# Optimization experiments

Hardware: AMD Instinct MI355X
Metric: run time of the kernel (lower is better)

## Reference

```python
import jax, jax.numpy as jnp
import numpy as np

D = 1024
H = 4
HD = D // H
B = 256
L = 64
DILATIONS = (1, 4, 8, 16)


def setup_inputs() -> dict:
    key = jax.random.key(0)
    ks = jax.random.split(key, 12)
    s = 1.0 / np.sqrt(D)
    return {
        "x": jax.random.normal(ks[0], (B, D), jnp.float32),
        "hist": jax.random.normal(ks[1], (L, B, D), jnp.float32),
        "Wq": jax.random.normal(ks[2], (D, D), jnp.float32) * s,
        "bq": jnp.zeros((D,), jnp.float32),
        "Wk": jax.random.normal(ks[3], (D, D), jnp.float32) * s,
        "bk": jnp.zeros((D,), jnp.float32),
        "Wv": jax.random.normal(ks[4], (D, D), jnp.float32) * s,
        "bv": jnp.zeros((D,), jnp.float32),
        "Wo": jax.random.normal(ks[5], (D, D), jnp.float32) * s,
        "bo": jnp.zeros((D,), jnp.float32),
        "dil_w": jnp.full((len(DILATIONS),), 1.0 / len(DILATIONS), jnp.float32),
        "gamma": jnp.ones((D,), jnp.float32),
        "beta": jnp.zeros((D,), jnp.float32),
    }


def reference(x, hist, Wq, bq, Wk, bk, Wv, bv, Wo, bo, dil_w, gamma, beta):
    scale = 1.0 / np.sqrt(HD)
    q = (x @ Wq + bq).reshape(B, H, HD)  # (B, H, HD)
    attended = []
    for d in DILATIONS:
        # history frames at stride d, concatenated along dim 0 (faithful to torch.cat)
        frames = hist[::d].reshape(-1, D)              # (T', D), T' = ceil(L/d)*B
        k = (frames @ Wk + bk).reshape(-1, H, HD)      # (T', H, HD)
        v = (frames @ Wv + bv).reshape(-1, H, HD)
        s = jnp.einsum('bhd,thd->bht', q, k) * scale   # (B, H, T')
        a = jax.nn.softmax(s, axis=-1)
        attended.append(jnp.einsum('bht,thd->bhd', a, v).reshape(B, D))
    w = jax.nn.softmax(dil_w, axis=0)
    combined = sum(w[i] * attended[i] for i in range(len(DILATIONS)))
    y = x + combined @ Wo + bo
    mu = jnp.mean(y, axis=-1, keepdims=True)
    var = jnp.var(y, axis=-1, keepdims=True)
    return (y - mu) / jnp.sqrt(var + 1e-5) * gamma + beta
```

## Files before the change

kernel.cpp:

```cpp
#include <hip/hip_runtime.h>


#define DD    1024
#define TALL  16384

typedef _Float16 half8  __attribute__((ext_vector_type(8)));
typedef _Float16 half4v __attribute__((ext_vector_type(4)));
typedef float    floatx4 __attribute__((ext_vector_type(4)));
typedef unsigned int u32;

static const size_t OFF_WOT  = 0;
static const size_t OFF_WV16 = 2097152;
static const size_t OFF_WK16 = 4194304;
static const size_t OFF_WQ16 = 6291456;
static const size_t OFF_XB   = 8388608;
static const size_t OFF_G    = 8912896;
static const size_t OFF_WVOT = 11010048;
static const size_t OFF_WQKT = 19398656;
static const size_t OFF_BVWO = 27787264;
static const size_t OFF_BQK  = 27791360;
static const size_t OFF_PHR  = 27807744;
static const size_t OFF_OPP  = 29904896;
static const size_t OFF_HB   = 38293504;
static const size_t OFF_HT   = 71848960;
static const size_t OFF_S    = 105403392;

__device__ __forceinline__ size_t chunk16_off(int g) {
  if (g < 4)  return (size_t)g * 2097152;
  if (g < 8)  return 19398656 + (size_t)(g - 4) * 2097152;
  if (g < 12) return 29904896 + (size_t)(g - 8) * 2097152;
  return 38293504 + (size_t)(g - 12) * 2097152;
}

__device__ __forceinline__ int frame_of(int g, int j) {
  if (g < 12) { int m = g * 4 + j; return m + m / 3 + 1; }
  if (g < 14) return 4 + 8 * ((g - 12) * 4 + j);
  if (g == 14) return 8 + 16 * j;
  return 16 * j;
}
__device__ __forceinline__ size_t foff(int g, int t) {
  return (size_t)frame_of(g, t >> 3) * 512 + (size_t)(t & 7) * 64;
}

__device__ __forceinline__ void gl_lds16(const void* g, void* l) {
  __builtin_amdgcn_global_load_lds((const __attribute__((address_space(1))) u32*)g,
                                   (__attribute__((address_space(3))) u32*)l, 16, 0, 0);
}

__global__ void prep_kernel(const float* __restrict__ Wo, const float* __restrict__ Wv,
                            const float* __restrict__ Wk, const float* __restrict__ Wq,
                            const float* __restrict__ x, const float* __restrict__ hist,
                            _Float16* __restrict__ WoT, _Float16* __restrict__ Wv16,
                            _Float16* __restrict__ Wk16, _Float16* __restrict__ Wq16,
                            _Float16* __restrict__ xb, _Float16* __restrict__ histb,
                            _Float16* __restrict__ histT) {
  int bid = blockIdx.x, tid = threadIdx.x;
  if (bid < 1024) {
    int k0 = (bid & 31) * 32, n0 = (bid >> 5) * 32;
    __shared__ float t32[32][33];
    int tx = tid & 31, ty = tid >> 5;
#pragma unroll
    for (int i = 0; i < 4; i++) {
      int r = ty + i * 8;
      t32[r][tx] = Wo[(size_t)(k0 + r) * DD + n0 + tx];
    }
    __syncthreads();
#pragma unroll
    for (int i = 0; i < 4; i++) {
      int r = ty + i * 8;
      WoT[(size_t)(n0 + r) * DD + k0 + tx] = (_Float16)t32[tx][r];
    }
  } else if (bid < 4352) {
    const float* src; _Float16* dst; size_t i;
    if (bid < 2048)      { src = Wv; dst = Wv16; i = (size_t)(bid - 1024) * 256 + tid; }
    else if (bid < 3072) { src = Wk; dst = Wk16; i = (size_t)(bid - 2048) * 256 + tid; }
    else if (bid < 4096) { src = Wq; dst = Wq16; i = (size_t)(bid - 3072) * 256 + tid; }
    else                 { src = x;  dst = xb;   i = (size_t)(bid - 4096) * 256 + tid; }
    float4 v = ((const float4*)src)[i];
    half4v h = {(_Float16)v.x, (_Float16)v.y, (_Float16)v.z, (_Float16)v.w};
    *(half4v*)(dst + 4 * i) = h;
  } else {
    int tb = bid - 4352;
    int t0 = (tb & 255) * 64, f0 = (tb >> 8) * 64;
    __shared__ _Float16 lt[64][72];
    int r = tid >> 2, c0 = (tid & 3) * 16;
    half8 s0, s1;
#pragma unroll
    for (int i = 0; i < 4; i++) {
      float4 v = *(const float4*)&hist[(size_t)(t0 + r) * 1024 + f0 + c0 + i * 4];
      half4v h = {(_Float16)v.x, (_Float16)v.y, (_Float16)v.z, (_Float16)v.w};
      *(half4v*)&lt[r][c0 + i * 4] = h;
      if (i < 2) { s0[i*4]=h[0]; s0[i*4+1]=h[1]; s0[i*4+2]=h[2]; s0[i*4+3]=h[3]; }
      else { s1[(i-2)*4]=h[0]; s1[(i-2)*4+1]=h[1]; s1[(i-2)*4+2]=h[2]; s1[(i-2)*4+3]=h[3]; }
    }
    *(half8*)&histb[(size_t)(t0 + r) * 1024 + f0 + c0] = s0;
    *(half8*)&histb[(size_t)(t0 + r) * 1024 + f0 + c0 + 8] = s1;
    __syncthreads();
    int fr = tid >> 2, tc0 = (tid & 3) * 16;
    half8 o0, o1;
#pragma unroll
    for (int j = 0; j < 8; j++) { o0[j] = lt[tc0 + j][fr]; o1[j] = lt[tc0 + 8 + j][fr]; }
    *(half8*)&histT[(size_t)(f0 + fr) * TALL + t0 + tc0] = o0;
    *(half8*)&histT[(size_t)(f0 + fr) * TALL + t0 + tc0 + 8] = o1;
  }
}

__device__ __forceinline__ void gemm_core(const _Float16* __restrict__ A, size_t lda,
                                          const _Float16* __restrict__ B, size_t ldb,
                                          int kIters, _Float16* As, _Float16* Bs,
                                          int tid, floatx4 acc[4][4]) {
  int lane = tid & 63, w = tid >> 6;
  int l15 = lane & 15, quad = lane >> 4;
  int wm = (w >> 1) * 64, wn = (w & 1) * 64;
  int swz = ((tid & 3) ^ ((tid >> 3) & 3)) * 8;
  int pch = (quad ^ ((l15 >> 1) & 3)) * 8;
  const char* gA0 = (const char*)(A + (size_t)(tid >> 2) * lda + swz);
  const char* gA1 = (const char*)(A + ((size_t)(tid >> 2) + 64) * lda + swz);
  const char* gB0 = (const char*)(B + (size_t)(tid >> 2) * ldb + swz);
  const char* gB1 = (const char*)(B + ((size_t)(tid >> 2) + 64) * ldb + swz);
  _Float16* lA = As + w * 512;
  _Float16* lB = Bs + w * 512;
#define GC_STAGE(buf, k)                                    \
  do {                                                      \
    size_t off_ = (size_t)(k) * 64;                         \
    gl_lds16(gA0 + off_, lA + (buf) * 4096);                \
    gl_lds16(gA1 + off_, lA + (buf) * 4096 + 2048);         \
    gl_lds16(gB0 + off_, lB + (buf) * 4096);                \
    gl_lds16(gB1 + off_, lB + (buf) * 4096 + 2048);         \
  } while (0)
#define GC_STEP(buf, k)                                                       \
  do {                                                                        \
    if ((k) + 1 < kIters) asm volatile("s_waitcnt vmcnt(4)" ::: "memory");    \
    else                  asm volatile("s_waitcnt vmcnt(0)" ::: "memory");    \
    asm volatile("s_barrier" ::: "memory");                                   \
    const _Float16* Ac_ = As + (buf) * 4096;                                  \
    const _Float16* Bc_ = Bs + (buf) * 4096;                                  \
    half8 a_[4];                                                              \
    _Pragma("unroll")                                                         \
    for (int mi = 0; mi < 4; mi++)                                            \
      a_[mi] = *(const half8*)&Ac_[(wm + mi * 16 + l15) * 32 + pch];          \
    _Pragma("unroll")                                                         \
    for (int ni = 0; ni < 4; ni++) {                                          \
      half8 b8_ = *(const half8*)&Bc_[(wn + ni * 16 + l15) * 32 + pch];       \
      _Pragma("unroll")                                                       \
      for (int mi = 0; mi < 4; mi++)                                          \
        acc[mi][ni] = __builtin_amdgcn_mfma_f32_16x16x32_f16(a_[mi], b8_,     \
                                                             acc[mi][ni], 0, 0, 0); \
    }                                                                         \
    asm volatile("s_waitcnt lgkmcnt(0)" ::: "memory");                        \
    asm volatile("s_barrier" ::: "memory");                                   \
    if ((k) + 2 < kIters) GC_STAGE(buf, (k) + 2);                             \
  } while (0)
  GC_STAGE(0, 0);
  GC_STAGE(1, 1);
  for (int kk = 0; kk < kIters; kk += 2) {
    GC_STEP(0, kk);
    GC_STEP(1, kk + 1);
  }
#undef GC_STEP
#undef GC_STAGE
}

__device__ __forceinline__ void gemm256_core(const _Float16* __restrict__ A, size_t lda,
                                             const _Float16* __restrict__ B, size_t ldb,
                                             int nT, _Float16* As, _Float16* Bs,
                                             int tid, floatx4 acc[8][4]) {
  int lane = tid & 63, w = tid >> 6;
  int l15 = lane & 15, quad = lane >> 4;
  int wr = w >> 2, wc = w & 3;
  int pch = (quad ^ ((l15 >> 1) & 3)) * 8;
  int srow = tid >> 2;
  int schunk = (tid & 3) ^ ((tid >> 3) & 3);
  const char* gA0 = (const char*)(A + (size_t)srow * lda + schunk * 8);
  const char* gA1 = (const char*)(A + (size_t)(srow + 128) * lda + schunk * 8);
  const char* gB0 = (const char*)(B + (size_t)srow * ldb + schunk * 8);
  const char* gB1 = (const char*)(B + (size_t)(srow + 128) * ldb + schunk * 8);
  _Float16* lA = As + w * 512;
  _Float16* lB = Bs + w * 512;
#define STA256(buf, t)                                        \
  do { size_t o_ = (size_t)(t) * 64;                          \
    gl_lds16(gA0 + o_, lA + (buf) * 8192);                    \
    gl_lds16(gA1 + o_, lA + (buf) * 8192 + 4096);             \
  } while (0)
#define STB256(buf, t)                                        \
  do { size_t o_ = (size_t)(t) * 64;                          \
    gl_lds16(gB0 + o_, lB + (buf) * 8192);                    \
    gl_lds16(gB1 + o_, lB + (buf) * 8192 + 4096);             \
  } while (0)
  STA256(0, 0); STB256(0, 0);
  if (nT > 1) { STA256(1, 1); STB256(1, 1); }
  if (nT > 2) { STA256(2, 2); STB256(2, 2); }
  for (int t = 0; t < nT; ++t) {
    int buf = t & 3;
    if (t + 2 < nT)      asm volatile("s_waitcnt vmcnt(8)" ::: "memory");
    else if (t + 1 < nT) asm volatile("s_waitcnt vmcnt(4)" ::: "memory");
    else                 asm volatile("s_waitcnt vmcnt(0)" ::: "memory");
    asm volatile("s_barrier" ::: "memory");
    const _Float16* Ac = As + buf * 8192;
    const _Float16* Bc = Bs + buf * 8192;
    half8 b8[4], a8[4];
#pragma unroll
    for (int ni = 0; ni < 4; ni++)
      b8[ni] = *(const half8*)&Bc[(wc * 64 + ni * 16 + l15) * 32 + pch];
#pragma unroll
    for (int mi = 0; mi < 4; mi++)
      a8[mi] = *(const half8*)&Ac[(wr * 128 + mi * 16 + l15) * 32 + pch];
    if (t + 3 < nT) STA256((t + 3) & 3, t + 3);
    asm volatile("s_barrier" ::: "memory");
    asm volatile("s_waitcnt lgkmcnt(0)" ::: "memory");
    __builtin_amdgcn_s_setprio(1);
#pragma unroll
    for (int mi = 0; mi < 4; mi++)
#pragma unroll
      for (int ni = 0; ni < 4; ni++)
        acc[mi][ni] = __builtin_amdgcn_mfma_f32_16x16x32_f16(a8[mi], b8[ni], acc[mi][ni], 0, 0, 0);
    __builtin_amdgcn_s_setprio(0);
    asm volatile("s_barrier" ::: "memory");
#pragma unroll
    for (int mi = 0; mi < 4; mi++)
      a8[mi] = *(const half8*)&Ac[(wr * 128 + 64 + mi * 16 + l15) * 32 + pch];
    if (t + 3 < nT) STB256((t + 3) & 3, t + 3);
    asm volatile("s_barrier" ::: "memory");
    asm volatile("s_waitcnt lgkmcnt(0)" ::: "memory");
    __builtin_amdgcn_s_setprio(1);
#pragma unroll
    for (int mi = 0; mi < 4; mi++)
#pragma unroll
      for (int ni = 0; ni < 4; ni++)
        acc[4 + mi][ni] = __builtin_amdgcn_mfma_f32_16x16x32_f16(a8[mi], b8[ni], acc[4 + mi][ni], 0, 0, 0);
    __builtin_amdgcn_s_setprio(0);
    asm volatile("s_barrier" ::: "memory");
  }
#undef STA256
#undef STB256
}

template <bool OUTF32>
__launch_bounds__(256, 3)
__global__ void gemm_f16_kernel(const _Float16* __restrict__ A, size_t lda, size_t aoffz,
                                const _Float16* __restrict__ B, size_t ldb, size_t boffz,
                                int kIters, const float* __restrict__ bias, size_t biasoffz,
                                float scale, void* __restrict__ C, size_t ldc, size_t coffz) {
  __shared__ __align__(16) _Float16 As[8192];
  __shared__ __align__(16) _Float16 Bs[8192];
  int tid = threadIdx.x;
  const _Float16* Ab = A + aoffz * blockIdx.z + (size_t)(blockIdx.y * 128) * lda;
  const _Float16* Bb = B + boffz * blockIdx.z + (size_t)(blockIdx.x * 128) * ldb;
  floatx4 acc[4][4];
  floatx4 zero = {0.f, 0.f, 0.f, 0.f};
#pragma unroll
  for (int a = 0; a < 4; a++)
#pragma unroll
    for (int b = 0; b < 4; b++) acc[a][b] = zero;
  gemm_core(Ab, lda, Bb, ldb, kIters, As, Bs, tid, acc);
  int lane = tid & 63, w = tid >> 6;
  int l15 = lane & 15, quad = lane >> 4;
  int wm = (w >> 1) * 64, wn = (w & 1) * 64;
#pragma unroll
  for (int mi = 0; mi < 4; mi++)
#pragma unroll
    for (int ni = 0; ni < 4; ni++) {
      int colg = blockIdx.x * 128 + wn + ni * 16 + l15;
      float bv = bias ? bias[biasoffz * blockIdx.z + colg] : 0.f;
#pragma unroll
      for (int r = 0; r < 4; r++) {
        int rowg = blockIdx.y * 128 + wm + mi * 16 + quad * 4 + r;
        float v = (acc[mi][ni][r] + bv) * scale;
        size_t idx = coffz * blockIdx.z + (size_t)rowg * ldc + colg;
        if (OUTF32) ((float*)C)[idx] = v;
        else ((_Float16*)C)[idx] = (_Float16)v;
      }
    }
}

__launch_bounds__(256, 3)
__global__ void wpack_kernel(const _Float16* __restrict__ WoT, const _Float16* __restrict__ Wv16,
                             const _Float16* __restrict__ Wk16, const _Float16* __restrict__ Wq16,
                             const float* __restrict__ bv, const float* __restrict__ bq,
                             _Float16* __restrict__ WVOT, _Float16* __restrict__ WQKT,
                             float* __restrict__ bvwo, float* __restrict__ bqk) {
  __shared__ __align__(16) _Float16 As[8192];
  __shared__ __align__(16) _Float16 Bs[8192];
  int bid = blockIdx.x, tid = threadIdx.x;
  if (bid < 512) {
    bool isQK = bid >= 256;
    int g = bid & 255;
    int x = g & 7, y = (g >> 3) & 7, z = g >> 6;
    const _Float16* A = isQK ? Wk16 : WoT;
    const _Float16* B = isQK ? Wq16 : Wv16;
    const _Float16* Ab = A + 256 * z + (size_t)(y * 128) * 1024;
    const _Float16* Bb = B + 256 * z + (size_t)(x * 128) * 1024;
    floatx4 acc[4][4];
    floatx4 zero = {0.f, 0.f, 0.f, 0.f};
#pragma unroll
    for (int a = 0; a < 4; a++)
#pragma unroll
      for (int b = 0; b < 4; b++) acc[a][b] = zero;
    gemm_core(Ab, 1024, Bb, 1024, 8, As, Bs, tid, acc);
    float scale = isQK ? 0.0625f : 1.0f;
    _Float16* C = isQK ? WQKT : WVOT;
    size_t ldc = isQK ? 1024 : 4096;
    size_t zoff = isQK ? (size_t)1048576 * z : (size_t)1024 * z;
    int lane = tid & 63, w = tid >> 6;
    int l15 = lane & 15, quad = lane >> 4;
    int wm = (w >> 1) * 64, wn = (w & 1) * 64;
#pragma unroll
    for (int mi = 0; mi < 4; mi++)
#pragma unroll
      for (int ni = 0; ni < 4; ni++) {
        int col = x * 128 + wn + ni * 16 + l15;
#pragma unroll
        for (int r = 0; r < 4; r++) {
          int row = y * 128 + wm + mi * 16 + quad * 4 + r;
          C[zoff + (size_t)row * ldc + col] = (_Float16)(acc[mi][ni][r] * scale);
        }
      }
  } else if (bid < 516) {
    int j = (bid - 512) * 256 + tid;
    const half8* row = (const half8*)(WoT + (size_t)j * 1024);
    float a = 0.f;
    for (int c = 0; c < 128; c++) {
      half8 w8 = row[c];
#pragma unroll
      for (int e = 0; e < 8; e++) a += bv[c * 8 + e] * (float)w8[e];
    }
    bvwo[j] = a;
  } else {
    int idx = (bid - 516) * 256 + tid;
    int h = idx >> 10, f = idx & 1023;
    const _Float16* row = Wk16 + (size_t)f * 1024 + h * 256;
    float a = 0.f;
    for (int n = 0; n < 256; n++) a += bq[h * 256 + n] * (float)row[n];
    bqk[idx] = a * 0.0625f;
  }
}

__launch_bounds__(512, 2)
__global__ void gemm256_s_kernel(const _Float16* __restrict__ G, const _Float16* __restrict__ histb,
                                 _Float16* __restrict__ Eout, float* __restrict__ zframe) {
  __shared__ __align__(16) _Float16 SM[65536];
  _Float16* As = SM;
  _Float16* Bs = SM + 32768;
  int bid = blockIdx.x, tid = threadIdx.x;
  int h = bid >> 6, nt = bid & 63;
  const _Float16* Ab = G + (size_t)h * 262144;
  const _Float16* Bb = histb + (size_t)(nt * 256) * 1024;
  floatx4 acc[8][4];
  floatx4 zero = {0.f, 0.f, 0.f, 0.f};
#pragma unroll
  for (int a = 0; a < 8; a++)
#pragma unroll
    for (int b = 0; b < 4; b++) acc[a][b] = zero;
  gemm256_core(Ab, 1024, Bb, 1024, 32, As, Bs, tid, acc);
  int lane = tid & 63, w = tid >> 6;
  int l15 = lane & 15, quad = lane >> 4;
  int wr = w >> 2, wc = w & 3;
  __syncthreads();
#pragma unroll
  for (int mh = 0; mh < 2; mh++)
#pragma unroll
    for (int mi = 0; mi < 4; mi++)
#pragma unroll
      for (int ni = 0; ni < 4; ni++) {
        int col = wc * 64 + ni * 16 + l15;
#pragma unroll
        for (int r = 0; r < 4; r++) {
          int row = wr * 128 + mh * 64 + mi * 16 + quad * 4 + r;
          int colsw = col ^ (((row >> 2) & 3) << 3);
          SM[row * 256 + colsw] = (_Float16)__expf(acc[mh * 4 + mi][ni][r]);
        }
      }
  __syncthreads();
  int c32 = lane & 31, hs = lane >> 5;
#pragma unroll
  for (int it = 0; it < 16; it++) {
    int row = w * 32 + it * 2 + hs;
    int cs = (c32 * 8) ^ (((row >> 2) & 3) << 3);
    half8 v = *(const half8*)&SM[row * 256 + cs];
    float s = 0.f;
#pragma unroll
    for (int j = 0; j < 8; j++) s += (float)v[j];
#pragma unroll
    for (int off = 1; off <= 16; off <<= 1) s += __shfl_xor(s, off, 64);
    *(half8*)&Eout[(size_t)h * 4194304 + (size_t)row * TALL + nt * 256 + c32 * 8] = v;
    if (c32 == 0) zframe[(size_t)(h * 256 + row) * 64 + nt] = s;
  }
}

__global__ void csoftmax_kernel(const float* __restrict__ zframe, const float* __restrict__ dil_w,
                                float* __restrict__ w4) {
  int row = blockIdx.x * 256 + threadIdx.x;
  const float* z = zframe + (size_t)row * 64;
  float z1 = 0.f, z4 = 0.f, z8 = 0.f, z16 = 0.f;
#pragma unroll
  for (int f = 0; f < 64; f++) {
    float v = z[f];
    z1 += v;
    if (!(f & 3))  z4 += v;
    if (!(f & 7))  z8 += v;
    if (!(f & 15)) z16 += v;
  }
  float w0 = dil_w[0], w1 = dil_w[1], w2 = dil_w[2], w3 = dil_w[3];
  float wmx = fmaxf(fmaxf(w0, w1), fmaxf(w2, w3));
  float e0 = __expf(w0 - wmx), e1 = __expf(w1 - wmx), e2 = __expf(w2 - wmx), e3 = __expf(w3 - wmx);
  float wsum = e0 + e1 + e2 + e3;
  float b0 = (e0 / wsum) / z1 * 256.0f;
  float b1 = (e1 / wsum) / z4 * 256.0f;
  float b2 = (e2 / wsum) / z8 * 256.0f;
  float b3 = (e3 / wsum) / z16 * 256.0f;
  float* wr = w4 + (size_t)row * 4;
  wr[0] = b0;
  wr[1] = b0 + b1;
  wr[2] = b0 + b1 + b2;
  wr[3] = b0 + b1 + b2 + b3;
}

__launch_bounds__(512, 2)
__global__ void gemm256_ph_kernel(const _Float16* __restrict__ E, const _Float16* __restrict__ histT,
                                  char* __restrict__ ws) {
  __shared__ __align__(16) _Float16 SM[65536];
  _Float16* As = SM;
  _Float16* Bs = SM + 32768;
  int bid = blockIdx.x, tid = threadIdx.x;
  int xcd = bid & 7, slot = bid >> 3;
  int g = xcd + 8 * (slot >> 4);
  int member = slot & 15;
  int h = member >> 2, nt = member & 3;
  int lane = tid & 63, w = tid >> 6;
  int l15 = lane & 15, quad = lane >> 4;
  int wr = w >> 2, wc = w & 3;
  int pch = (quad ^ ((l15 >> 1) & 3)) * 8;
  int srow = tid >> 2;
  int schunk = (tid & 3) ^ ((tid >> 3) & 3);
  const _Float16* A = E + (size_t)h * 4194304;
  const _Float16* B = histT + (size_t)(nt * 256) * TALL;
  const char* gA0 = (const char*)(A + (size_t)srow * TALL + schunk * 8);
  const char* gA1 = (const char*)(A + (size_t)(srow + 128) * TALL + schunk * 8);
  const char* gB0 = (const char*)(B + (size_t)srow * TALL + schunk * 8);
  const char* gB1 = (const char*)(B + (size_t)(srow + 128) * TALL + schunk * 8);
  _Float16* lA = As + w * 512;
  _Float16* lB = Bs + w * 512;
  floatx4 acc[8][4];
  floatx4 zero = {0.f, 0.f, 0.f, 0.f};
#pragma unroll
  for (int a = 0; a < 8; a++)
#pragma unroll
    for (int b = 0; b < 4; b++) acc[a][b] = zero;
#define PSTA(buf, t)                                          \
  do { size_t o_ = foff(g, t);                                \
    gl_lds16(gA0 + o_, lA + (buf) * 8192);                    \
    gl_lds16(gA1 + o_, lA + (buf) * 8192 + 4096);             \
  } while (0)
#define PSTB(buf, t)                                          \
  do { size_t o_ = foff(g, t);                                \
    gl_lds16(gB0 + o_, lB + (buf) * 8192);                    \
    gl_lds16(gB1 + o_, lB + (buf) * 8192 + 4096);             \
  } while (0)
  PSTA(0, 0); PSTB(0, 0);
  PSTA(1, 1); PSTB(1, 1);
  PSTA(2, 2); PSTB(2, 2);
  for (int t = 0; t < 32; ++t) {
    int buf = t & 3;
    if (t + 2 < 32)      asm volatile("s_waitcnt vmcnt(8)" ::: "memory");
    else if (t + 1 < 32) asm volatile("s_waitcnt vmcnt(4)" ::: "memory");
    else                 asm volatile("s_waitcnt vmcnt(0)" ::: "memory");
    asm volatile("s_barrier" ::: "memory");
    const _Float16* Ac = As + buf * 8192;
    const _Float16* Bc = Bs + buf * 8192;
    half8 b8[4], a8[4];
#pragma unroll
    for (int ni = 0; ni < 4; ni++)
      b8[ni] = *(const half8*)&Bc[(wc * 64 + ni * 16 + l15) * 32 + pch];
#pragma unroll
    for (int mi = 0; mi < 4; mi++)
      a8[mi] = *(const half8*)&Ac[(wr * 128 + mi * 16 + l15) * 32 + pch];
    if (t + 3 < 32) PSTA((t + 3) & 3, t + 3);
    asm volatile("s_barrier" ::: "memory");
    asm volatile("s_waitcnt lgkmcnt(0)" ::: "memory");
    __builtin_amdgcn_s_setprio(1);
#pragma unroll
    for (int mi = 0; mi < 4; mi++)
#pragma unroll
      for (int ni = 0; ni < 4; ni++)
        acc[mi][ni] = __builtin_amdgcn_mfma_f32_16x16x32_f16(a8[mi], b8[ni], acc[mi][ni], 0, 0, 0);
    __builtin_amdgcn_s_setprio(0);
    asm volatile("s_barrier" ::: "memory");
#pragma unroll
    for (int mi = 0; mi < 4; mi++)
      a8[mi] = *(const half8*)&Ac[(wr * 128 + 64 + mi * 16 + l15) * 32 + pch];
    if (t + 3 < 32) PSTB((t + 3) & 3, t + 3);
    asm volatile("s_barrier" ::: "memory");
    asm volatile("s_waitcnt lgkmcnt(0)" ::: "memory");
    __builtin_amdgcn_s_setprio(1);
#pragma unroll
    for (int mi = 0; mi < 4; mi++)
#pragma unroll
      for (int ni = 0; ni < 4; ni++)
        acc[4 + mi][ni] = __builtin_amdgcn_mfma_f32_16x16x32_f16(a8[mi], b8[ni], acc[4 + mi][ni], 0, 0, 0);
    __builtin_amdgcn_s_setprio(0);
    asm volatile("s_barrier" ::: "memory");
  }
#undef PSTA
#undef PSTB
  __syncthreads();
#pragma unroll
  for (int mh = 0; mh < 2; mh++)
#pragma unroll
    for (int mi = 0; mi < 4; mi++)
#pragma unroll
      for (int ni = 0; ni < 4; ni++) {
        int col = wc * 64 + ni * 16 + l15;
#pragma unroll
        for (int r = 0; r < 4; r++) {
          int row = wr * 128 + mh * 64 + mi * 16 + quad * 4 + r;
          int colsw = col ^ (((row >> 2) & 3) << 3);
          SM[row * 256 + colsw] = (_Float16)acc[mh * 4 + mi][ni][r];
        }
      }
  __syncthreads();
  _Float16* chunk = (_Float16*)(ws + chunk16_off(g));
  int c32 = lane & 31, hs = lane >> 5;
  int colbase = h * 1024 + nt * 256;
#pragma unroll
  for (int it = 0; it < 16; it++) {
    int row = w * 32 + it * 2 + hs;
    int cs = (c32 * 8) ^ (((row >> 2) & 3) << 3);
    half8 v = *(const half8*)&SM[row * 256 + cs];
    *(half8*)&chunk[(size_t)row * 4096 + colbase + c32 * 8] = v;
  }
}

__global__ void reduce_ph_kernel(const char* __restrict__ ws, const float* __restrict__ w4,
                                 _Float16* __restrict__ PHred) {
  size_t e8 = ((size_t)blockIdx.x * 256 + threadIdx.x) * 8;
  int q = (int)(e8 >> 12);
  int h = (int)((e8 >> 10) & 3);
  const float* wr = w4 + (size_t)(h * 256 + q) * 4;
  float sA[8] = {0,0,0,0,0,0,0,0}, sB[8] = {0,0,0,0,0,0,0,0};
  float sC[8] = {0,0,0,0,0,0,0,0}, sD[8] = {0,0,0,0,0,0,0,0};
#pragma unroll
  for (int g = 0; g < 12; g++) {
    const _Float16* p = (const _Float16*)(ws + chunk16_off(g));
    half8 v = *(const half8*)&p[e8];
#pragma unroll
    for (int j = 0; j < 8; j++) sA[j] += (float)v[j];
  }
#pragma unroll
  for (int g = 12; g < 14; g++) {
    const _Float16* p = (const _Float16*)(ws + chunk16_off(g));
    half8 v = *(const half8*)&p[e8];
#pragma unroll
    for (int j = 0; j < 8; j++) sB[j] += (float)v[j];
  }
  {
    const _Float16* p = (const _Float16*)(ws + chunk16_off(14));
    half8 v = *(const half8*)&p[e8];
#pragma unroll
    for (int j = 0; j < 8; j++) sC[j] += (float)v[j];
  }
  {
    const _Float16* p = (const _Float16*)(ws + chunk16_off(15));
    half8 v = *(const half8*)&p[e8];
#pragma unroll
    for (int j = 0; j < 8; j++) sD[j] += (float)v[j];
  }
  float wA = wr[0], wB = wr[1], wC = wr[2], wD = wr[3];
  half8 o;
#pragma unroll
  for (int j = 0; j < 8; j++)
    o[j] = (_Float16)(wA * sA[j] + wB * sB[j] + wC * sC[j] + wD * sD[j]);
  *(half8*)&PHred[e8] = o;
}

__global__ void ln_kernel(const float* __restrict__ x, const float* __restrict__ part2,
                          const float* __restrict__ bo, const float* __restrict__ bvwo,
                          const float* __restrict__ gamma, const float* __restrict__ beta,
                          float* __restrict__ out) {
  int b = blockIdx.x, t = threadIdx.x;
  __shared__ float red[8];
  float y[4];
  float sum = 0.f, sq = 0.f;
#pragma unroll
  for (int i = 0; i < 4; i++) {
    int j = t + i * 256;
    float v = x[(size_t)b * 1024 + j] + bo[j] + bvwo[j];
#pragma unroll
    for (int z = 0; z < 8; z++) v += part2[(size_t)z * 262144 + (size_t)b * 1024 + j];
    y[i] = v;
    sum += v;
    sq += v * v;
  }
#pragma unroll
  for (int off = 1; off < 64; off <<= 1) {
    sum += __shfl_xor(sum, off, 64);
    sq += __shfl_xor(sq, off, 64);
  }
  int w = t >> 6, lane = t & 63;
  if (lane == 0) { red[w] = sum; red[4 + w] = sq; }
  __syncthreads();
  sum = red[0] + red[1] + red[2] + red[3];
  sq = red[4] + red[5] + red[6] + red[7];
  float mu = sum * (1.f / 1024.f);
  float var = sq * (1.f / 1024.f) - mu * mu;
  float inv = rsqrtf(var + 1e-5f);
#pragma unroll
  for (int i = 0; i < 4; i++) {
    int j = t + i * 256;
    out[(size_t)b * 1024 + j] = (y[i] - mu) * inv * gamma[j] + beta[j];
  }
}

extern "C" void kernel_launch(void* const* d_in, const int* in_sizes, int n_in,
                              void* d_out, int out_size, void* d_ws, size_t ws_size,
                              hipStream_t stream) {
  const float* x     = (const float*)d_in[0];
  const float* hist  = (const float*)d_in[1];
  const float* Wq    = (const float*)d_in[2];
  const float* bq    = (const float*)d_in[3];
  const float* Wk    = (const float*)d_in[4];
  const float* Wv    = (const float*)d_in[6];
  const float* bv    = (const float*)d_in[7];
  const float* Wo    = (const float*)d_in[8];
  const float* bo    = (const float*)d_in[9];
  const float* dil_w = (const float*)d_in[10];
  const float* gamma = (const float*)d_in[11];
  const float* beta  = (const float*)d_in[12];
  char* ws = (char*)d_ws;

  _Float16* WoT   = (_Float16*)(ws + OFF_WOT);
  _Float16* Wv16  = (_Float16*)(ws + OFF_WV16);
  _Float16* Wk16  = (_Float16*)(ws + OFF_WK16);
  _Float16* Wq16  = (_Float16*)(ws + OFF_WQ16);
  _Float16* xb    = (_Float16*)(ws + OFF_XB);
  _Float16* G     = (_Float16*)(ws + OFF_G);
  _Float16* WVOT  = (_Float16*)(ws + OFF_WVOT);
  _Float16* WQKT  = (_Float16*)(ws + OFF_WQKT);
  float* bvwo     = (float*)(ws + OFF_BVWO);
  float* bqk      = (float*)(ws + OFF_BQK);
  _Float16* PHred = (_Float16*)(ws + OFF_PHR);
  float* oppart   = (float*)(ws + OFF_OPP);
  _Float16* histb = (_Float16*)(ws + OFF_HB);
  _Float16* histT = (_Float16*)(ws + OFF_HT);
  _Float16* Eb    = (_Float16*)(ws + OFF_S);
  float* zframe   = (float*)(ws + OFF_WQKT);
  float* w4       = (float*)(ws + OFF_G);

  prep_kernel<<<dim3(8448), 256, 0, stream>>>(Wo, Wv, Wk, Wq, x, hist,
                                              WoT, Wv16, Wk16, Wq16, xb, histb, histT);
  wpack_kernel<<<dim3(532), 256, 0, stream>>>(WoT, Wv16, Wk16, Wq16, bv, bq,
                                              WVOT, WQKT, bvwo, bqk);
  gemm_f16_kernel<false><<<dim3(8, 2, 4), 256, 0, stream>>>(
      xb, 1024, 0, WQKT, 1024, 1048576, 32, bqk, 1024, 1.0f, (void*)G, 1024, 262144);
  gemm256_s_kernel<<<dim3(256), 512, 0, stream>>>(G, histb, Eb, zframe);
  csoftmax_kernel<<<dim3(4), 256, 0, stream>>>(zframe, dil_w, w4);
  gemm256_ph_kernel<<<dim3(256), 512, 0, stream>>>(Eb, histT, ws);
  reduce_ph_kernel<<<dim3(512), 256, 0, stream>>>(ws, w4, PHred);
  gemm_f16_kernel<true><<<dim3(8, 2, 8), 256, 0, stream>>>(
      PHred, 4096, 512, WVOT, 4096, 512, 16, nullptr, 0, 1.0f / 256.0f,
      (void*)oppart, 1024, 262144);
  ln_kernel<<<dim3(256), 256, 0, stream>>>(x, oppart, bo, bvwo, gamma, beta, (float*)d_out);
}
```

Measured before the change: 309.7 us.

## Double-buffer LDS fragment reads across k-tiles and cut barriers in 256x256 GEMM mainloop

Replaces the per-tile loop, which used four barriers and two lgkmcnt(0) waits, with a software-pipelined loop. The next tile's A/B fragments are read from LDS into a second register set while the current tile's MFMAs run, and all four global->LDS loads for a future tile are issued in one batch. The same templated core, with a pluggable offset functor, is now shared by the plain GEMM and the strided-history kernel. The goal is to hide LDS latency behind MFMA and drop barrier stalls, at the cost of more live VGPRs (five fragment sets), which may hurt occupancy or cause spills under launch_bounds(256,3).

Result: slower. 318.0 us (+2.7%).

```diff
diff --git a/kernel.cpp b/kernel.cpp
--- a/kernel.cpp
+++ b/kernel.cpp
@@ -41,6 +41,9 @@
 __device__ __forceinline__ size_t foff(int g, int t) {
   return (size_t)frame_of(g, t >> 3) * 512 + (size_t)(t & 7) * 64;
 }
+
+struct LinOff { __device__ __forceinline__ size_t operator()(int t) const { return (size_t)t * 64; } };
+struct ClsOff { int g; __device__ __forceinline__ size_t operator()(int t) const { return foff(g, t); } };
 
 __device__ __forceinline__ void gl_lds16(const void* g, void* l) {
   __builtin_amdgcn_global_load_lds((const __attribute__((address_space(1))) u32*)g,
@@ -161,9 +164,10 @@
 #undef GC_STAGE
 }
 
-__device__ __forceinline__ void gemm256_core(const _Float16* __restrict__ A, size_t lda,
+template <typename OFF>
+__device__ __forceinline__ void gemm256_pipe(const _Float16* __restrict__ A, size_t lda,
                                              const _Float16* __restrict__ B, size_t ldb,
-                                             int nT, _Float16* As, _Float16* Bs,
+                                             OFF off, _Float16* As, _Float16* Bs,
                                              int tid, floatx4 acc[8][4]) {
   int lane = tid & 63, w = tid >> 6;
   int l15 = lane & 15, quad = lane >> 4;
@@ -177,62 +181,72 @@
   const char* gB1 = (const char*)(B + (size_t)(srow + 128) * ldb + schunk * 8);
   _Float16* lA = As + w * 512;
   _Float16* lB = Bs + w * 512;
-#define STA256(buf, t)                                        \
-  do { size_t o_ = (size_t)(t) * 64;                          \
+  half8 B0[4], A0[4], B1[4], A1[4], Ah[4];
+#define P_ST(buf, t)                                          \
+  do { size_t o_ = off(t);                                    \
     gl_lds16(gA0 + o_, lA + (buf) * 8192);                    \
     gl_lds16(gA1 + o_, lA + (buf) * 8192 + 4096);             \
-  } while (0)
-#define STB256(buf, t)                                        \
-  do { size_t o_ = (size_t)(t) * 64;                          \
     gl_lds16(gB0 + o_, lB + (buf) * 8192);                    \
     gl_lds16(gB1 + o_, lB + (buf) * 8192 + 4096);             \
   } while (0)
-  STA256(0, 0); STB256(0, 0);
-  if (nT > 1) { STA256(1, 1); STB256(1, 1); }
-  if (nT > 2) { STA256(2, 2); STB256(2, 2); }
-  for (int t = 0; t < nT; ++t) {
-    int buf = t & 3;
-    if (t + 2 < nT)      asm volatile("s_waitcnt vmcnt(8)" ::: "memory");
-    else if (t + 1 < nT) asm volatile("s_waitcnt vmcnt(4)" ::: "memory");
-    else                 asm volatile("s_waitcnt vmcnt(0)" ::: "memory");
-    asm volatile("s_barrier" ::: "memory");
-    const _Float16* Ac = As + buf * 8192;
-    const _Float16* Bc = Bs + buf * 8192;
-    half8 b8[4], a8[4];
-#pragma unroll
-    for (int ni = 0; ni < 4; ni++)
-      b8[ni] = *(const half8*)&Bc[(wc * 64 + ni * 16 + l15) * 32 + pch];
-#pragma unroll
-    for (int mi = 0; mi < 4; mi++)
-      a8[mi] = *(const half8*)&Ac[(wr * 128 + mi * 16 + l15) * 32 + pch];
-    if (t + 3 < nT) STA256((t + 3) & 3, t + 3);
-    asm volatile("s_barrier" ::: "memory");
-    asm volatile("s_waitcnt lgkmcnt(0)" ::: "memory");
-    __builtin_amdgcn_s_setprio(1);
-#pragma unroll
-    for (int mi = 0; mi < 4; mi++)
-#pragma unroll
-      for (int ni = 0; ni < 4; ni++)
-        acc[mi][ni] = __builtin_amdgcn_mfma_f32_16x16x32_f16(a8[mi], b8[ni], acc[mi][ni], 0, 0, 0);
-    __builtin_amdgcn_s_setprio(0);
-    asm volatile("s_barrier" ::: "memory");
-#pragma unroll
-    for (int mi = 0; mi < 4; mi++)
-      a8[mi] = *(const half8*)&Ac[(wr * 128 + 64 + mi * 16 + l15) * 32 + pch];
-    if (t + 3 < nT) STB256((t + 3) & 3, t + 3);
-    asm volatile("s_barrier" ::: "memory");
-    asm volatile("s_waitcnt lgkmcnt(0)" ::: "memory");
-    __builtin_amdgcn_s_setprio(1);
-#pragma unroll
-    for (int mi = 0; mi < 4; mi++)
-#pragma unroll
-      for (int ni = 0; ni < 4; ni++)
-        acc[4 + mi][ni] = __builtin_amdgcn_mfma_f32_16x16x32_f16(a8[mi], b8[ni], acc[4 + mi][ni], 0, 0, 0);
-    __builtin_amdgcn_s_setprio(0);
-    asm volatile("s_barrier" ::: "memory");
-  }
-#undef STA256
-#undef STB256
+#define P_RDM(BN, AN, buf)                                                     \
+  do {                                                                         \
+    const _Float16* Ac_ = As + (buf) * 8192;                                   \
+    const _Float16* Bc_ = Bs + (buf) * 8192;                                   \
+    _Pragma("unroll")                                                          \
+    for (int ni = 0; ni < 4; ni++)                                             \
+      BN[ni] = *(const half8*)&Bc_[(wc * 64 + ni * 16 + l15) * 32 + pch];      \
+    _Pragma("unroll")                                                          \
+    for (int mi = 0; mi < 4; mi++)                                             \
+      AN[mi] = *(const half8*)&Ac_[(wr * 128 + mi * 16 + l15) * 32 + pch];     \
+  } while (0)
+#define P_RDH(buf)                                                             \
+  do {                                                                         \
+    const _Float16* Ac_ = As + (buf) * 8192;                                   \
+    _Pragma("unroll")                                                          \
+    for (int mi = 0; mi < 4; mi++)                                             \
+      Ah[mi] = *(const half8*)&Ac_[(wr * 128 + 64 + mi * 16 + l15) * 32 + pch];\
+  } while (0)
+#define P_MM(CB, CA)                                                           \
+  do {                                                                         \
+    __builtin_amdgcn_s_setprio(1);                                             \
+    _Pragma("unroll")                                                          \
+    for (int mi = 0; mi < 4; mi++)                                             \
+      _Pragma("unroll")                                                        \
+      for (int ni = 0; ni < 4; ni++)                                           \
+        acc[mi][ni] = __builtin_amdgcn_mfma_f32_16x16x32_f16(CA[mi], CB[ni], acc[mi][ni], 0, 0, 0); \
+    _Pragma("unroll")                                                          \
+    for (int mi = 0; mi < 4; mi++)                                             \
+      _Pragma("unroll")                                                        \
+      for (int ni = 0; ni < 4; ni++)                                           \
+        acc[4 + mi][ni] = __builtin_amdgcn_mfma_f32_16x16x32_f16(Ah[mi], CB[ni], acc[4 + mi][ni], 0, 0, 0); \
+    __builtin_amdgcn_s_setprio(0);                                             \
+  } while (0)
+#define P_STEP(CB, CA, NB, NA, t)                                              \
+  do {                                                                         \
+    P_RDH((t) & 3);                                                            \
+    if ((t) + 1 < 32) {                                                        \
+      if ((t) + 2 < 32) asm volatile("s_waitcnt vmcnt(4)" ::: "memory");       \
+      else              asm volatile("s_waitcnt vmcnt(0)" ::: "memory");       \
+      asm volatile("s_barrier" ::: "memory");                                  \
+      P_RDM(NB, NA, ((t) + 1) & 3);                                            \
+      if ((t) + 3 < 32) P_ST(((t) + 3) & 3, (t) + 3);                          \
+    }                                                                          \
+    P_MM(CB, CA);                                                              \
+  } while (0)
+  P_ST(0, 0); P_ST(1, 1); P_ST(2, 2);
+  asm volatile("s_waitcnt vmcnt(8)" ::: "memory");
+  asm volatile("s_barrier" ::: "memory");
+  P_RDM(B0, A0, 0);
+  for (int t = 0; t < 32; t += 2) {
+    P_STEP(B0, A0, B1, A1, t);
+    P_STEP(B1, A1, B0, A0, t + 1);
+  }
+#undef P_STEP
+#undef P_MM
+#undef P_RDH
+#undef P_RDM
+#undef P_ST
 }
 
 template <bool OUTF32>
@@ -351,7 +365,7 @@
   for (int a = 0; a < 8; a++)
 #pragma unroll
     for (int b = 0; b < 4; b++) acc[a][b] = zero;
-  gemm256_core(Ab, 1024, Bb, 1024, 32, As, Bs, tid, acc);
+  gemm256_pipe(Ab, 1024, Bb, 1024, LinOff{}, As, Bs, tid, acc);
   int lane = tid & 63, w = tid >> 6;
   int l15 = lane & 15, quad = lane >> 4;
   int wr = w >> 2, wc = w & 3;
@@ -426,82 +440,18 @@
   int g = xcd + 8 * (slot >> 4);
   int member = slot & 15;
   int h = member >> 2, nt = member & 3;
+  const _Float16* A = E + (size_t)h * 4194304;
+  const _Float16* B = histT + (size_t)(nt * 256) * TALL;
+  floatx4 acc[8][4];
+  floatx4 zero = {0.f, 0.f, 0.f, 0.f};
+#pragma unroll
+  for (int a = 0; a < 8; a++)
+#pragma unroll
+    for (int b = 0; b < 4; b++) acc[a][b] = zero;
+  gemm256_pipe(A, TALL, B, TALL, ClsOff{g}, As, Bs, tid, acc);
   int lane = tid & 63, w = tid >> 6;
   int l15 = lane & 15, quad = lane >> 4;
   int wr = w >> 2, wc = w & 3;
-  int pch = (quad ^ ((l15 >> 1) & 3)) * 8;
-  int srow = tid >> 2;
-  int schunk = (tid & 3) ^ ((tid >> 3) & 3);
-  const _Float16* A = E + (size_t)h * 4194304;
-  const _Float16* B = histT + (size_t)(nt * 256) * TALL;
-  const char* gA0 = (const char*)(A + (size_t)srow * TALL + schunk * 8);
-  const char* gA1 = (const char*)(A + (size_t)(srow + 128) * TALL + schunk * 8);
-  const char* gB0 = (const char*)(B + (size_t)srow * TALL + schunk * 8);
-  const char* gB1 = (const char*)(B + (size_t)(srow + 128) * TALL + schunk * 8);
-  _Float16* lA = As + w * 512;
-  _Float16* lB = Bs + w * 512;
-  floatx4 acc[8][4];
-  floatx4 zero = {0.f, 0.f, 0.f, 0.f};
-#pragma unroll
-  for (int a = 0; a < 8; a++)
-#pragma unroll
-    for (int b = 0; b < 4; b++) acc[a][b] = zero;
-#define PSTA(buf, t)                                          \
-  do { size_t o_ = foff(g, t);                                \
-    gl_lds16(gA0 + o_, lA + (buf) * 8192);                    \
-    gl_lds16(gA1 + o_, lA + (buf) * 8192 + 4096);             \
-  } while (0)
-#define PSTB(buf, t)                                          \
-  do { size_t o_ = foff(g, t);                                \
-    gl_lds16(gB0 + o_, lB + (buf) * 8192);                    \
-    gl_lds16(gB1 + o_, lB + (buf) * 8192 + 4096);             \
-  } while (0)
-  PSTA(0, 0); PSTB(0, 0);
-  PSTA(1, 1); PSTB(1, 1);
-  PSTA(2, 2); PSTB(2, 2);
-  for (int t = 0; t < 32; ++t) {
-    int buf = t & 3;
-    if (t + 2 < 32)      asm volatile("s_waitcnt vmcnt(8)" ::: "memory");
-    else if (t + 1 < 32) asm volatile("s_waitcnt vmcnt(4)" ::: "memory");
-    else                 asm volatile("s_waitcnt vmcnt(0)" ::: "memory");
-    asm volatile("s_barrier" ::: "memory");
-    const _Float16* Ac = As + buf * 8192;
-    const _Float16* Bc = Bs + buf * 8192;
-    half8 b8[4], a8[4];
-#pragma unroll
-    for (int ni = 0; ni < 4; ni++)
-      b8[ni] = *(const half8*)&Bc[(wc * 64 + ni * 16 + l15) * 32 + pch];
-#pragma unroll
-    for (int mi = 0; mi < 4; mi++)
-      a8[mi] = *(const half8*)&Ac[(wr * 128 + mi * 16 + l15) * 32 + pch];
-    if (t + 3 < 32) PSTA((t + 3) & 3, t + 3);
-    asm volatile("s_barrier" ::: "memory");
-    asm volatile("s_waitcnt lgkmcnt(0)" ::: "memory");
-    __builtin_amdgcn_s_setprio(1);
-#pragma unroll
-    for (int mi = 0; mi < 4; mi++)
-#pragma unroll
-      for (int ni = 0; ni < 4; ni++)
-        acc[mi][ni] = __builtin_amdgcn_mfma_f32_16x16x32_f16(a8[mi], b8[ni], acc[mi][ni], 0, 0, 0);
-    __builtin_amdgcn_s_setprio(0);
-    asm volatile("s_barrier" ::: "memory");
-#pragma unroll
-    for (int mi = 0; mi < 4; mi++)
-      a8[mi] = *(const half8*)&Ac[(wr * 128 + 64 + mi * 16 + l15) * 32 + pch];
-    if (t + 3 < 32) PSTB((t + 3) & 3, t + 3);
-    asm volatile("s_barrier" ::: "memory");
-    asm volatile("s_waitcnt lgkmcnt(0)" ::: "memory");
-    __builtin_amdgcn_s_setprio(1);
-#pragma unroll
-    for (int mi = 0; mi < 4; mi++)
-#pragma unroll
-      for (int ni = 0; ni < 4; ni++)
-        acc[4 + mi][ni] = __builtin_amdgcn_mfma_f32_16x16x32_f16(a8[mi], b8[ni], acc[4 + mi][ni], 0, 0, 0);
-    __builtin_amdgcn_s_setprio(0);
-    asm volatile("s_barrier" ::: "memory");
-  }
-#undef PSTA
-#undef PSTB
   __syncthreads();
 #pragma unroll
   for (int mh = 0; mh < 2; mh++)
```

## Split-K the small G and output GEMMs and fold channel softmax into PH kernel

Applied to the files above, without the earlier changes.

The G projection GEMM (64 blocks) becomes a 4-way split-K kernel writing fp32 partials, followed by a new reduction kernel that adds the bias and converts to fp16. The output GEMM doubles its split-K from 8 to 16 slices, and the layer-norm kernel now sums 16 partials. The separate 4-block channel-softmax kernel is removed and its work moved into an extra block of the PH GEMM launch. The PH main loop now reuses a templated shared GEMM core. The aim is to fill more CUs in the small GEMMs and drop one launch, at the cost of extra partial-sum memory traffic and one added reduce launch.

After: 302.6 us. 2.3% less time.

```diff
diff --git a/kernel.cpp b/kernel.cpp
--- a/kernel.cpp
+++ b/kernel.cpp
@@ -161,10 +161,11 @@
 #undef GC_STAGE
 }
 
-__device__ __forceinline__ void gemm256_core(const _Float16* __restrict__ A, size_t lda,
-                                             const _Float16* __restrict__ B, size_t ldb,
-                                             int nT, _Float16* As, _Float16* Bs,
-                                             int tid, floatx4 acc[8][4]) {
+template <typename OFF>
+__device__ __forceinline__ void gemm256_run(const _Float16* __restrict__ A, size_t lda,
+                                            const _Float16* __restrict__ B, size_t ldb,
+                                            OFF off, _Float16* As, _Float16* Bs,
+                                            int tid, floatx4 acc[8][4]) {
   int lane = tid & 63, w = tid >> 6;
   int l15 = lane & 15, quad = lane >> 4;
   int wr = w >> 2, wc = w & 3;
@@ -177,23 +178,23 @@
   const char* gB1 = (const char*)(B + (size_t)(srow + 128) * ldb + schunk * 8);
   _Float16* lA = As + w * 512;
   _Float16* lB = Bs + w * 512;
-#define STA256(buf, t)                                        \
-  do { size_t o_ = (size_t)(t) * 64;                          \
+#define PSTA(buf, t)                                          \
+  do { size_t o_ = off(t);                                    \
     gl_lds16(gA0 + o_, lA + (buf) * 8192);                    \
     gl_lds16(gA1 + o_, lA + (buf) * 8192 + 4096);             \
   } while (0)
-#define STB256(buf, t)                                        \
-  do { size_t o_ = (size_t)(t) * 64;                          \
+#define PSTB(buf, t)                                          \
+  do { size_t o_ = off(t);                                    \
     gl_lds16(gB0 + o_, lB + (buf) * 8192);                    \
     gl_lds16(gB1 + o_, lB + (buf) * 8192 + 4096);             \
   } while (0)
-  STA256(0, 0); STB256(0, 0);
-  if (nT > 1) { STA256(1, 1); STB256(1, 1); }
-  if (nT > 2) { STA256(2, 2); STB256(2, 2); }
-  for (int t = 0; t < nT; ++t) {
+  PSTA(0, 0); PSTB(0, 0);
+  PSTA(1, 1); PSTB(1, 1);
+  PSTA(2, 2); PSTB(2, 2);
+  for (int t = 0; t < 32; ++t) {
     int buf = t & 3;
-    if (t + 2 < nT)      asm volatile("s_waitcnt vmcnt(8)" ::: "memory");
-    else if (t + 1 < nT) asm volatile("s_waitcnt vmcnt(4)" ::: "memory");
+    if (t + 2 < 32)      asm volatile("s_waitcnt vmcnt(8)" ::: "memory");
+    else if (t + 1 < 32) asm volatile("s_waitcnt vmcnt(4)" ::: "memory");
     else                 asm volatile("s_waitcnt vmcnt(0)" ::: "memory");
     asm volatile("s_barrier" ::: "memory");
     const _Float16* Ac = As + buf * 8192;
@@ -205,7 +206,7 @@
 #pragma unroll
     for (int mi = 0; mi < 4; mi++)
       a8[mi] = *(const half8*)&Ac[(wr * 128 + mi * 16 + l15) * 32 + pch];
-    if (t + 3 < nT) STA256((t + 3) & 3, t + 3);
+    if (t + 3 < 32) PSTA((t + 3) & 3, t + 3);
     asm volatile("s_barrier" ::: "memory");
     asm volatile("s_waitcnt lgkmcnt(0)" ::: "memory");
     __builtin_amdgcn_s_setprio(1);
@@ -219,7 +220,7 @@
 #pragma unroll
     for (int mi = 0; mi < 4; mi++)
       a8[mi] = *(const half8*)&Ac[(wr * 128 + 64 + mi * 16 + l15) * 32 + pch];
-    if (t + 3 < nT) STB256((t + 3) & 3, t + 3);
+    if (t + 3 < 32) PSTB((t + 3) & 3, t + 3);
     asm volatile("s_barrier" ::: "memory");
     asm volatile("s_waitcnt lgkmcnt(0)" ::: "memory");
     __builtin_amdgcn_s_setprio(1);
@@ -231,9 +232,12 @@
     __builtin_amdgcn_s_setprio(0);
     asm volatile("s_barrier" ::: "memory");
   }
-#undef STA256
-#undef STB256
-}
+#undef PSTA
+#undef PSTB
+}
+
+struct LinOff { __device__ __forceinline__ size_t operator()(int t) const { return (size_t)t * 64; } };
+struct ClsOff { int g; __device__ __forceinline__ size_t operator()(int t) const { return foff(g, t); } };
 
 template <bool OUTF32>
 __launch_bounds__(256, 3)
@@ -271,6 +275,54 @@
         else ((_Float16*)C)[idx] = (_Float16)v;
       }
     }
+}
+
+__launch_bounds__(256, 3)
+__global__ void gemm_g_kernel(const _Float16* __restrict__ xb, const _Float16* __restrict__ WQKT,
+                              float* __restrict__ gpart) {
+  __shared__ __align__(16) _Float16 As[8192];
+  __shared__ __align__(16) _Float16 Bs[8192];
+  int tid = threadIdx.x;
+  int z = blockIdx.z, sp = z >> 2, h = z & 3;
+  const _Float16* Ab = xb + sp * 256 + (size_t)(blockIdx.y * 128) * 1024;
+  const _Float16* Bb = WQKT + (size_t)h * 1048576 + sp * 256 + (size_t)(blockIdx.x * 128) * 1024;
+  floatx4 acc[4][4];
+  floatx4 zero = {0.f, 0.f, 0.f, 0.f};
+#pragma unroll
+  for (int a = 0; a < 4; a++)
+#pragma unroll
+    for (int b = 0; b < 4; b++) acc[a][b] = zero;
+  gemm_core(Ab, 1024, Bb, 1024, 8, As, Bs, tid, acc);
+  int lane = tid & 63, w = tid >> 6;
+  int l15 = lane & 15, quad = lane >> 4;
+  int wm = (w >> 1) * 64, wn = (w & 1) * 64;
+#pragma unroll
+  for (int mi = 0; mi < 4; mi++)
+#pragma unroll
+    for (int ni = 0; ni < 4; ni++) {
+      int col = blockIdx.x * 128 + wn + ni * 16 + l15;
+#pragma unroll
+      for (int r = 0; r < 4; r++) {
+        int row = blockIdx.y * 128 + wm + mi * 16 + quad * 4 + r;
+        gpart[(size_t)z * 262144 + (size_t)row * 1024 + col] = acc[mi][ni][r];
+      }
+    }
+}
+
+__global__ void reduce_g_kernel(const float* __restrict__ gpart, const float* __restrict__ bqk,
+                                _Float16* __restrict__ G) {
+  size_t e4 = ((size_t)blockIdx.x * 256 + threadIdx.x) * 4;
+  int h = (int)(e4 >> 18);
+  size_t rem = e4 & 262143;
+  int d = (int)(e4 & 1023);
+  float4 s = *(const float4*)&bqk[h * 1024 + d];
+#pragma unroll
+  for (int sp = 0; sp < 4; sp++) {
+    float4 p = *(const float4*)&gpart[(size_t)(sp * 4 + h) * 262144 + rem];
+    s.x += p.x; s.y += p.y; s.z += p.z; s.w += p.w;
+  }
+  half4v o = {(_Float16)s.x, (_Float16)s.y, (_Float16)s.z, (_Float16)s.w};
+  *(half4v*)&G[e4] = o;
 }
 
 __launch_bounds__(256, 3)
@@ -351,7 +403,7 @@
   for (int a = 0; a < 8; a++)
 #pragma unroll
     for (int b = 0; b < 4; b++) acc[a][b] = zero;
-  gemm256_core(Ab, 1024, Bb, 1024, 32, As, Bs, tid, acc);
+  gemm256_run(Ab, 1024, Bb, 1024, LinOff{}, As, Bs, tid, acc);
   int lane = tid & 63, w = tid >> 6;
   int l15 = lane & 15, quad = lane >> 4;
   int wr = w >> 2, wc = w & 3;
@@ -387,121 +439,60 @@
   }
 }
 
-__global__ void csoftmax_kernel(const float* __restrict__ zframe, const float* __restrict__ dil_w,
-                                float* __restrict__ w4) {
-  int row = blockIdx.x * 256 + threadIdx.x;
-  const float* z = zframe + (size_t)row * 64;
-  float z1 = 0.f, z4 = 0.f, z8 = 0.f, z16 = 0.f;
-#pragma unroll
-  for (int f = 0; f < 64; f++) {
-    float v = z[f];
-    z1 += v;
-    if (!(f & 3))  z4 += v;
-    if (!(f & 7))  z8 += v;
-    if (!(f & 15)) z16 += v;
-  }
-  float w0 = dil_w[0], w1 = dil_w[1], w2 = dil_w[2], w3 = dil_w[3];
-  float wmx = fmaxf(fmaxf(w0, w1), fmaxf(w2, w3));
-  float e0 = __expf(w0 - wmx), e1 = __expf(w1 - wmx), e2 = __expf(w2 - wmx), e3 = __expf(w3 - wmx);
-  float wsum = e0 + e1 + e2 + e3;
-  float b0 = (e0 / wsum) / z1 * 256.0f;
-  float b1 = (e1 / wsum) / z4 * 256.0f;
-  float b2 = (e2 / wsum) / z8 * 256.0f;
-  float b3 = (e3 / wsum) / z16 * 256.0f;
-  float* wr = w4 + (size_t)row * 4;
-  wr[0] = b0;
-  wr[1] = b0 + b1;
-  wr[2] = b0 + b1 + b2;
-  wr[3] = b0 + b1 + b2 + b3;
-}
-
 __launch_bounds__(512, 2)
 __global__ void gemm256_ph_kernel(const _Float16* __restrict__ E, const _Float16* __restrict__ histT,
-                                  char* __restrict__ ws) {
+                                  const float* __restrict__ zframe, const float* __restrict__ dil_w,
+                                  float* __restrict__ w4, char* __restrict__ ws) {
   __shared__ __align__(16) _Float16 SM[65536];
+  int bid = blockIdx.x, tid = threadIdx.x;
+  if (bid == 256) {
+    float w0 = dil_w[0], w1 = dil_w[1], w2 = dil_w[2], w3 = dil_w[3];
+    float wmx = fmaxf(fmaxf(w0, w1), fmaxf(w2, w3));
+    float e0 = __expf(w0 - wmx), e1 = __expf(w1 - wmx), e2 = __expf(w2 - wmx), e3 = __expf(w3 - wmx);
+    float wsum = e0 + e1 + e2 + e3;
+#pragma unroll
+    for (int i = 0; i < 2; i++) {
+      int row = i * 512 + tid;
+      const float* z = zframe + (size_t)row * 64;
+      float z1 = 0.f, z4 = 0.f, z8 = 0.f, z16 = 0.f;
+#pragma unroll
+      for (int f = 0; f < 64; f++) {
+        float v = z[f];
+        z1 += v;
+        if (!(f & 3))  z4 += v;
+        if (!(f & 7))  z8 += v;
+        if (!(f & 15)) z16 += v;
+      }
+      float b0 = (e0 / wsum) / z1 * 256.0f;
+      float b1 = (e1 / wsum) / z4 * 256.0f;
+      float b2 = (e2 / wsum) / z8 * 256.0f;
+      float b3 = (e3 / wsum) / z16 * 256.0f;
+      float* wr = w4 + (size_t)row * 4;
+      wr[0] = b0;
+      wr[1] = b0 + b1;
+      wr[2] = b0 + b1 + b2;
+      wr[3] = b0 + b1 + b2 + b3;
+    }
+    return;
+  }
   _Float16* As = SM;
   _Float16* Bs = SM + 32768;
-  int bid = blockIdx.x, tid = threadIdx.x;
   int xcd = bid & 7, slot = bid >> 3;
   int g = xcd + 8 * (slot >> 4);
   int member = slot & 15;
   int h = member >> 2, nt = member & 3;
+  const _Float16* A = E + (size_t)h * 4194304;
+  const _Float16* B = histT + (size_t)(nt * 256) * TALL;
+  floatx4 acc[8][4];
+  floatx4 zero = {0.f, 0.f, 0.f, 0.f};
+#pragma unroll
+  for (int a = 0; a < 8; a++)
+#pragma unroll
+    for (int b = 0; b < 4; b++) acc[a][b] = zero;
+  gemm256_run(A, TALL, B, TALL, ClsOff{g}, As, Bs, tid, acc);
   int lane = tid & 63, w = tid >> 6;
   int l15 = lane & 15, quad = lane >> 4;
   int wr = w >> 2, wc = w & 3;
-  int pch = (quad ^ ((l15 >> 1) & 3)) * 8;
-  int srow = tid >> 2;
-  int schunk = (tid & 3) ^ ((tid >> 3) & 3);
-  const _Float16* A = E + (size_t)h * 4194304;
-  const _Float16* B = histT + (size_t)(nt * 256) * TALL;
-  const char* gA0 = (const char*)(A + (size_t)srow * TALL + schunk * 8);
-  const char* gA1 = (const char*)(A + (size_t)(srow + 128) * TALL + schunk * 8);
-  const char* gB0 = (const char*)(B + (size_t)srow * TALL + schunk * 8);
-  const char* gB1 = (const char*)(B + (size_t)(srow + 128) * TALL + schunk * 8);
-  _Float16* lA = As + w * 512;
-  _Float16* lB = Bs + w * 512;
-  floatx4 acc[8][4];
-  floatx4 zero = {0.f, 0.f, 0.f, 0.f};
-#pragma unroll
-  for (int a = 0; a < 8; a++)
-#pragma unroll
-    for (int b = 0; b < 4; b++) acc[a][b] = zero;
-#define PSTA(buf, t)                                          \
-  do { size_t o_ = foff(g, t);                                \
-    gl_lds16(gA0 + o_, lA + (buf) * 8192);                    \
-    gl_lds16(gA1 + o_, lA + (buf) * 8192 + 4096);             \
-  } while (0)
-#define PSTB(buf, t)                                          \
-  do { size_t o_ = foff(g, t);                                \
-    gl_lds16(gB0 + o_, lB + (buf) * 8192);                    \
-    gl_lds16(gB1 + o_, lB + (buf) * 8192 + 4096);             \
-  } while (0)
-  PSTA(0, 0); PSTB(0, 0);
-  PSTA(1, 1); PSTB(1, 1);
-  PSTA(2, 2); PSTB(2, 2);
-  for (int t = 0; t < 32; ++t) {
-    int buf = t & 3;
-    if (t + 2 < 32)      asm volatile("s_waitcnt vmcnt(8)" ::: "memory");
-    else if (t + 1 < 32) asm volatile("s_waitcnt vmcnt(4)" ::: "memory");
-    else                 asm volatile("s_waitcnt vmcnt(0)" ::: "memory");
-    asm volatile("s_barrier" ::: "memory");
-    const _Float16* Ac = As + buf * 8192;
-    const _Float16* Bc = Bs + buf * 8192;
-    half8 b8[4], a8[4];
-#pragma unroll
-    for (int ni = 0; ni < 4; ni++)
-      b8[ni] = *(const half8*)&Bc[(wc * 64 + ni * 16 + l15) * 32 + pch];
-#pragma unroll
-    for (int mi = 0; mi < 4; mi++)
-      a8[mi] = *(const half8*)&Ac[(wr * 128 + mi * 16 + l15) * 32 + pch];
-    if (t + 3 < 32) PSTA((t + 3) & 3, t + 3);
-    asm volatile("s_barrier" ::: "memory");
-    asm volatile("s_waitcnt lgkmcnt(0)" ::: "memory");
-    __builtin_amdgcn_s_setprio(1);
-#pragma unroll
-    for (int mi = 0; mi < 4; mi++)
-#pragma unroll
-      for (int ni = 0; ni < 4; ni++)
-        acc[mi][ni] = __builtin_amdgcn_mfma_f32_16x16x32_f16(a8[mi], b8[ni], acc[mi][ni], 0, 0, 0);
-    __builtin_amdgcn_s_setprio(0);
-    asm volatile("s_barrier" ::: "memory");
-#pragma unroll
-    for (int mi = 0; mi < 4; mi++)
-      a8[mi] = *(const half8*)&Ac[(wr * 128 + 64 + mi * 16 + l15) * 32 + pch];
-    if (t + 3 < 32) PSTB((t + 3) & 3, t + 3);
-    asm volatile("s_barrier" ::: "memory");
-    asm volatile("s_waitcnt lgkmcnt(0)" ::: "memory");
-    __builtin_amdgcn_s_setprio(1);
-#pragma unroll
-    for (int mi = 0; mi < 4; mi++)
-#pragma unroll
-      for (int ni = 0; ni < 4; ni++)
-        acc[4 + mi][ni] = __builtin_amdgcn_mfma_f32_16x16x32_f16(a8[mi], b8[ni], acc[4 + mi][ni], 0, 0, 0);
-    __builtin_amdgcn_s_setprio(0);
-    asm volatile("s_barrier" ::: "memory");
-  }
-#undef PSTA
-#undef PSTB
   __syncthreads();
 #pragma unroll
   for (int mh = 0; mh < 2; mh++)
@@ -585,7 +576,7 @@
     int j = t + i * 256;
     float v = x[(size_t)b * 1024 + j] + bo[j] + bvwo[j];
 #pragma unroll
-    for (int z = 0; z < 8; z++) v += part2[(size_t)z * 262144 + (size_t)b * 1024 + j];
+    for (int z = 0; z < 16; z++) v += part2[(size_t)z * 262144 + (size_t)b * 1024 + j];
     y[i] = v;
     sum += v;
     sq += v * v;
@@ -642,21 +633,21 @@
   _Float16* histb = (_Float16*)(ws + OFF_HB);
   _Float16* histT = (_Float16*)(ws + OFF_HT);
   _Float16* Eb    = (_Float16*)(ws + OFF_S);
-  float* zframe   = (float*)(ws + OFF_WQKT);
+  float* gpart    = (float*)(ws + OFF_S);
+  float* zframe   = (float*)(ws + OFF_PHR);
   float* w4       = (float*)(ws + OFF_G);
 
   prep_kernel<<<dim3(8448), 256, 0, stream>>>(Wo, Wv, Wk, Wq, x, hist,
                                               WoT, Wv16, Wk16, Wq16, xb, histb, histT);
   wpack_kernel<<<dim3(532), 256, 0, stream>>>(WoT, Wv16, Wk16, Wq16, bv, bq,
                                               WVOT, WQKT, bvwo, bqk);
-  gemm_f16_kernel<false><<<dim3(8, 2, 4), 256, 0, stream>>>(
-      xb, 1024, 0, WQKT, 1024, 1048576, 32, bqk, 1024, 1.0f, (void*)G, 1024, 262144);
+  gemm_g_kernel<<<dim3(8, 2, 16), 256, 0, stream>>>(xb, WQKT, gpart);
+  reduce_g_kernel<<<dim3(1024), 256, 0, stream>>>(gpart, bqk, G);
   gemm256_s_kernel<<<dim3(256), 512, 0, stream>>>(G, histb, Eb, zframe);
-  csoftmax_kernel<<<dim3(4), 256, 0, stream>>>(zframe, dil_w, w4);
-  gemm256_ph_kernel<<<dim3(256), 512, 0, stream>>>(Eb, histT, ws);
+  gemm256_ph_kernel<<<dim3(257), 512, 0, stream>>>(Eb, histT, zframe, dil_w, w4, ws);
   reduce_ph_kernel<<<dim3(512), 256, 0, stream>>>(ws, w4, PHred);
-  gemm_f16_kernel<true><<<dim3(8, 2, 8), 256, 0, stream>>>(
-      PHred, 4096, 512, WVOT, 4096, 512, 16, nullptr, 0, 1.0f / 256.0f,
+  gemm_f16_kernel<true><<<dim3(8, 2, 16), 256, 0, stream>>>(
+      PHred, 4096, 256, WVOT, 4096, 256, 8, nullptr, 0, 1.0f / 256.0f,
       (void*)oppart, 1024, 262144);
   ln_kernel<<<dim3(256), 256, 0, stream>>>(x, oppart, bo, bvwo, gamma, beta, (float*)d_out);
 }
```
